# Kernel tuning notes

Measured on AMD Instinct MI355X. Metric: run time of the kernel, lower is better.

The kernel has to match this reference:

```python
import jax, jax.numpy as jnp
import numpy as np

# Model hyperparams (match init_kwargs)
B, T, CIN, COUT = 4, 12, 4, 4
P = 16; HIMG = WIMG = 256; HP = WP = 16
D = 384; L = 4; DFF = 4 * D; MAXG = 0.3
CPLX = jnp.complex64

# NOTE: RiemannianCliffordConv2d / TemporalPropagator / FluxTracker / basis /
# encoder / decoder sources were not provided; they are reconstructed here as
# faithful-structure surrogates: plain conv2d for the Clifford conv, complex
# linear eigen-basis encode/decode, exp-decay scan operators, complex FFN,
# patch-embed conv encoder and per-patch linear decoder. sde_mode='ode' so the
# stochastic branch is skipped, matching the explicit guard in the source.

def _ln(x, g, b):
    m = x.mean(-1, keepdims=True)
    v = jnp.var(x, axis=-1, keepdims=True)
    return (x - m) * jax.lax.rsqrt(v + 1e-5) * g + b

def _conv(x, w, b, stride, pad):
    y = jax.lax.conv_general_dilated(x, w, (stride, stride), pad,
                                     dimension_numbers=('NCHW', 'OIHW', 'NCHW'))
    return y + b[None, :, None, None]

def _pscan(A, X):
    # first-order linear recurrence h_t = A_t*h_{t-1} + X_t via associative scan over axis=1
    def comb(l, r):
        al, xl = l; ar, xr = r
        return al * ar, xl * ar + xr
    return jax.lax.associative_scan(comb, (A, X), axis=1)[1]

def _cgelu(z):
    return jax.nn.gelu(z.real) + 1j * jax.nn.gelu(z.imag)

def _model(x, dt, enc_w, enc_b, ns_g, ns_b, cw, cb, nt_g, nt_b,
           E_re, E_im, Ei_re, Ei_im, lam_flux, Ws_re, Ws_im, Wg, nu, omega,
           w1_re, w1_im, w2_re, w2_im, dec_w, dec_b):
    Bx, Tx = x.shape[0], x.shape[1]
    # ---- encoder: patch-embed conv -> complex latent (B,T,D,HP,WP)
    xf = x.reshape(Bx * Tx, CIN, HIMG, WIMG)
    e = _conv(xf, enc_w, enc_b, P, 'VALID')              # (BT, 2D, HP, WP)
    zr, zi = jnp.split(e, 2, axis=1)
    z = (zr + 1j * zi).astype(CPLX).reshape(Bx, Tx, D, HP, WP)
    for i in range(L):
        E = E_re[i] + 1j * E_im[i]
        Ei = Ei_re[i] + 1j * Ei_im[i]
        Ws = Ws_re[i] + 1j * Ws_im[i]
        W1 = w1_re[i] + 1j * w1_im[i]
        W2 = w2_re[i] + 1j * w2_im[i]
        # ---- _apply_spatial (residual Clifford conv on stacked re/im)
        xflat = z.reshape(Bx * Tx, D, HP, WP)
        xr2 = jnp.concatenate([xflat.real, xflat.imag], axis=1)   # (BT,2D,H,W)
        xn = jnp.transpose(xr2, (0, 2, 3, 1))
        xn = _ln(xn, ns_g[i], ns_b[i])
        xn = jnp.transpose(xn, (0, 3, 1, 2))
        xs = _conv(xn, cw[i], cb[i], 1, 'SAME')
        sre, sim = jnp.split(xs, 2, axis=1)
        xflat = xflat + (sre + 1j * sim)
        z = xflat.reshape(Bx, Tx, D, HP, WP)
        # ---- eigen-basis encode
        xp = jnp.transpose(z, (0, 1, 3, 4, 2))                    # (B,T,H,W,D)
        x_eig = jnp.einsum('bthwd,de->bthwe', xp, E)
        x_mean = x_eig.mean(axis=(2, 3))                          # (B,T,D)
        # ---- flux tracker scan (states start at zero => flux_prev term vanishes)
        a = jnp.exp(-jax.nn.softplus(lam_flux[i])[None, None] * dt[..., None])
        A_flux = a.astype(CPLX)
        X_flux = x_mean * dt[..., None]
        flux = _pscan(A_flux, X_flux)                             # (B,T,D) complex
        source = jnp.einsum('btd,de->bte', flux, Ws)
        gate = jax.nn.sigmoid(flux.real * Wg[i][None, None])      # (B,T,D) real
        g = gate[:, :, None, None, :]
        forcing = x_eig * g + source[:, :, None, None, :] * (1.0 - g)
        # ---- transition operators and temporal pscan
        lam = jnp.clip(-jax.nn.softplus(nu[i]), -5.0, MAXG) + 1j * omega[i]  # (D,)
        op_decay = jnp.exp(lam[None, None] * dt[..., None])       # (B,T,D) complex
        op_forcing = (op_decay - 1.0) / lam
        u_t = forcing * op_forcing[:, :, None, None, :]           # (B,T,H,W,D)
        # h_prev is zero-initialized per _init_states => its t0 contribution is zero
        A_full = jnp.broadcast_to(op_decay[:, :, None, None, :], u_t.shape)
        u_out = _pscan(A_full, u_t)                               # (B,T,H,W,D)
        # ---- decode + temporal FFN residual
        decoded = jnp.einsum('bthwd,de->bthwe', u_out, Ei)
        dec5 = jnp.transpose(decoded, (0, 1, 4, 2, 3))            # (B,T,D,H,W)
        df = dec5.reshape(Bx * Tx, D, HP, WP)
        dr = jnp.concatenate([df.real, df.imag], axis=1)
        dn = _ln(jnp.transpose(dr, (0, 2, 3, 1)), nt_g[i], nt_b[i])
        dn = jnp.transpose(dn, (0, 3, 1, 2))
        nre, nim = jnp.split(dn, 2, axis=1)
        xcl = jnp.transpose(nre + 1j * nim, (0, 2, 3, 1))          # (BT,H,W,D)
        delta = jnp.einsum('bhwf,fd->bhwd', _cgelu(jnp.einsum('bhwd,df->bhwf', xcl, W1)), W2)
        delta = jnp.transpose(delta, (0, 3, 1, 2))
        x_out = (df + delta).reshape(Bx, Tx, D, HP, WP)
        z = z + x_out
    # ---- ensemble decoder (mean member): per-patch linear head + depth-to-space
    feats = jnp.concatenate([z.real, z.imag], axis=2)             # (B,T,2D,H,W)
    fl = jnp.transpose(feats, (0, 1, 3, 4, 2))                    # (B,T,H,W,2D)
    y = jnp.einsum('bthwc,oc->bthwo', fl, dec_w) + dec_b
    y = y.reshape(Bx, Tx, HP, WP, COUT, P, P)
    y = jnp.transpose(y, (0, 1, 4, 2, 5, 3, 6)).reshape(Bx, Tx, COUT, HP * P, WP * P)
    return y


def setup_inputs() -> dict:
    key = jax.random.key(0)
    ks = jax.random.split(key, 32)
    s = 0.02
    d = {}
    d['x'] = jax.random.normal(ks[0], (B, T, CIN, HIMG, WIMG), dtype=jnp.float32)
    d['dt'] = jax.random.uniform(ks[1], (B, T), minval=0.5, maxval=1.5, dtype=jnp.float32)
    d['enc_w'] = jax.random.normal(ks[2], (2 * D, CIN, P, P), dtype=jnp.float32) * s
    d['enc_b'] = jnp.zeros((2 * D,), jnp.float32)
    d['ns_g'] = jnp.ones((L, 2 * D), jnp.float32)
    d['ns_b'] = jnp.zeros((L, 2 * D), jnp.float32)
    d['cw'] = jax.random.normal(ks[3], (L, 2 * D, 2 * D, 3, 3), dtype=jnp.float32) * s
    d['cb'] = jnp.zeros((L, 2 * D), jnp.float32)
    d['nt_g'] = jnp.ones((L, 2 * D), jnp.float32)
    d['nt_b'] = jnp.zeros((L, 2 * D), jnp.float32)
    d['E_re'] = jax.random.normal(ks[4], (L, D, D), dtype=jnp.float32) * s
    d['E_im'] = jax.random.normal(ks[5], (L, D, D), dtype=jnp.float32) * s
    d['Ei_re'] = jax.random.normal(ks[6], (L, D, D), dtype=jnp.float32) * s
    d['Ei_im'] = jax.random.normal(ks[7], (L, D, D), dtype=jnp.float32) * s
    d['lam_flux'] = jax.random.normal(ks[8], (L, D), dtype=jnp.float32)
    d['Ws_re'] = jax.random.normal(ks[9], (L, D, D), dtype=jnp.float32) * s
    d['Ws_im'] = jax.random.normal(ks[10], (L, D, D), dtype=jnp.float32) * s
    d['Wg'] = jax.random.normal(ks[11], (L, D), dtype=jnp.float32)
    d['nu'] = jax.random.normal(ks[12], (L, D), dtype=jnp.float32)
    d['omega'] = jax.random.normal(ks[13], (L, D), dtype=jnp.float32) * 0.5
    d['w1_re'] = jax.random.normal(ks[14], (L, D, DFF), dtype=jnp.float32) * s
    d['w1_im'] = jax.random.normal(ks[15], (L, D, DFF), dtype=jnp.float32) * s
    d['w2_re'] = jax.random.normal(ks[16], (L, DFF, D), dtype=jnp.float32) * s
    d['w2_im'] = jax.random.normal(ks[17], (L, DFF, D), dtype=jnp.float32) * s
    d['dec_w'] = jax.random.normal(ks[18], (COUT * P * P, 2 * D), dtype=jnp.float32) * s
    d['dec_b'] = jnp.zeros((COUT * P * P,), jnp.float32)
    return d


def reference(x, dt, enc_w, enc_b, ns_g, ns_b, cw, cb, nt_g, nt_b,
              E_re, E_im, Ei_re, Ei_im, lam_flux, Ws_re, Ws_im, Wg, nu, omega,
              w1_re, w1_im, w2_re, w2_im, dec_w, dec_b):
    return _model(x, dt, enc_w, enc_b, ns_g, ns_b, cw, cb, nt_g, nt_b,
                  E_re, E_im, Ei_re, Ei_im, lam_flux, Ws_re, Ws_im, Wg, nu, omega,
                  w1_re, w1_im, w2_re, w2_im, dec_w, dec_b)
```

## Files before the change

### kernel.cpp

```cpp
#include <hip/hip_runtime.h>
#include <cstddef>
#include <cstdint>

typedef unsigned short u16;
typedef short bf16x8 __attribute__((ext_vector_type(8)));
typedef float f32x4 __attribute__((ext_vector_type(4)));

__device__ __forceinline__ float gelu_tanh(float x) {
  float x3 = x * x * x;
  float t = tanhf(0.7978845608028654f * (x + 0.044715f * x3));
  return 0.5f * x * (1.0f + t);
}
__device__ __forceinline__ float softplus_f(float x) {
  return (x > 20.0f) ? x : log1pf(expf(x));
}
__device__ __forceinline__ u16 f2bf(float f) {
  uint32_t u = __float_as_uint(f);
  uint32_t r = (u + 0x7fffu + ((u >> 16) & 1u)) >> 16;
  return (u16)r;
}

__device__ __forceinline__ void gload16(const u16* g, u16* l) {
  __builtin_amdgcn_global_load_lds(
      (const __attribute__((address_space(1))) void*)g,
      (__attribute__((address_space(3))) void*)l, 16, 0, 0);
}

template <int MODE>
__global__ __launch_bounds__(256) void gemm128_kernel(
    const u16* __restrict__ A, const u16* __restrict__ Bt, int K, int ldc,
    float* __restrict__ Cf, u16* __restrict__ Cb, const float* __restrict__ bias) {
  __shared__ u16 As[128 * 32];
  __shared__ u16 Bs[128 * 32];
  const int m0 = blockIdx.x * 128, n0 = blockIdx.y * 128;
  const int tid = threadIdx.x;
  const int lane = tid & 63, w = tid >> 6;
  const int lane15 = lane & 15, quad = lane >> 4;
  const int r0 = lane >> 2, e0 = (lane & 3) * 8;

  const u16* ag0 = A + (size_t)(m0 + w * 32 + r0) * K + e0;
  const u16* ag1 = A + (size_t)(m0 + w * 32 + 16 + r0) * K + e0;
  const u16* bg0 = Bt + (size_t)(n0 + w * 32 + r0) * K + e0;
  const u16* bg1 = Bt + (size_t)(n0 + w * 32 + 16 + r0) * K + e0;
  u16* As0 = As + w * 1024; u16* As1 = As0 + 512;
  u16* Bs0 = Bs + w * 1024; u16* Bs1 = Bs0 + 512;

  f32x4 acc[4][4] = {};
  const int wy = w >> 1, wx = w & 1;
  const int ar_base = (wy * 64 + lane15) * 32 + quad * 8;
  const int br_base = (wx * 64 + lane15) * 32 + quad * 8;

  for (int k0 = 0; k0 < K; k0 += 32) {
    gload16(ag0 + k0, As0);
    gload16(ag1 + k0, As1);
    gload16(bg0 + k0, Bs0);
    gload16(bg1 + k0, Bs1);
    __syncthreads();
    bf16x8 af[4], bf[4];
#pragma unroll
    for (int i = 0; i < 4; ++i) af[i] = *(const bf16x8*)&As[ar_base + i * 16 * 32];
#pragma unroll
    for (int j = 0; j < 4; ++j) bf[j] = *(const bf16x8*)&Bs[br_base + j * 16 * 32];
#pragma unroll
    for (int i = 0; i < 4; ++i)
#pragma unroll
      for (int j = 0; j < 4; ++j)
        acc[i][j] = __builtin_amdgcn_mfma_f32_16x16x32_bf16(af[i], bf[j], acc[i][j], 0, 0, 0);
    __syncthreads();
  }

  const int mw = m0 + wy * 64, nw = n0 + wx * 64;
#pragma unroll
  for (int i = 0; i < 4; ++i) {
#pragma unroll
    for (int j = 0; j < 4; ++j) {
      const int col = nw + j * 16 + lane15;
#pragma unroll
      for (int r = 0; r < 4; ++r) {
        const int row = mw + i * 16 + quad * 4 + r;
        const float v = acc[i][j][r];
        if (MODE == 0) {
          Cf[(size_t)row * ldc + col] = v;
        } else if (MODE == 1) {
          Cb[(size_t)row * ldc + col] = f2bf(gelu_tanh(v));
        } else if (MODE == 2) {
          Cf[(size_t)row * ldc + col] += v;
        } else if (MODE == 3) {
          const int frame = row >> 8, pix = row & 255;
          const int hp = pix >> 4, wp = pix & 15;
          const int co = col >> 8, p1 = (col >> 4) & 15, p2 = col & 15;
          Cf[(((size_t)frame * 4 + co) * 256 + hp * 16 + p1) * 256 + wp * 16 + p2] = v + bias[col];
        }
      }
    }
  }
}

__global__ __launch_bounds__(256) void conv_mfma128_kernel(
    const u16* __restrict__ xnp, const u16* __restrict__ Btc,
    const float* __restrict__ cbias,
    float* __restrict__ z, u16* __restrict__ zb) {
  __shared__ u16 As[128 * 32];
  __shared__ u16 Bs[128 * 32];
  const int m0 = blockIdx.x * 128, n0 = blockIdx.y * 128;
  const int tid = threadIdx.x;
  const int lane = tid & 63, w = tid >> 6;
  const int lane15 = lane & 15, quad = lane >> 4;
  const int r0 = lane >> 2, e0 = (lane & 3) * 8;

  const int rowA0 = m0 + w * 32 + r0, rowA1 = rowA0 + 16;
  const long long cen0 = ((long long)(rowA0 >> 8) * 324 + ((((rowA0 & 255) >> 4) + 1) * 18) + (rowA0 & 15) + 1) * 768 + e0;
  const long long cen1 = ((long long)(rowA1 >> 8) * 324 + ((((rowA1 & 255) >> 4) + 1) * 18) + (rowA1 & 15) + 1) * 768 + e0;
  const u16* bg0 = Btc + (size_t)(n0 + w * 32 + r0) * 6912 + e0;
  const u16* bg1 = bg0 + (size_t)16 * 6912;
  u16* As0 = As + w * 1024; u16* As1 = As0 + 512;
  u16* Bs0 = Bs + w * 1024; u16* Bs1 = Bs0 + 512;

  f32x4 acc[4][4] = {};
  const int wy = w >> 1, wx = w & 1;
  const int ar_base = (wy * 64 + lane15) * 32 + quad * 8;
  const int br_base = (wx * 64 + lane15) * 32 + quad * 8;

  for (int tap = 0; tap < 9; ++tap) {
    const int doff = ((tap / 3 - 1) * 18 + (tap % 3 - 1)) * 768;
    const u16* a0 = xnp + cen0 + doff;
    const u16* a1 = xnp + cen1 + doff;
    const u16* b0 = bg0 + tap * 768;
    const u16* b1 = bg1 + tap * 768;
    for (int kc = 0; kc < 768; kc += 32) {
      gload16(a0 + kc, As0);
      gload16(a1 + kc, As1);
      gload16(b0 + kc, Bs0);
      gload16(b1 + kc, Bs1);
      __syncthreads();
      bf16x8 af[4], bf[4];
#pragma unroll
      for (int i = 0; i < 4; ++i) af[i] = *(const bf16x8*)&As[ar_base + i * 16 * 32];
#pragma unroll
      for (int j = 0; j < 4; ++j) bf[j] = *(const bf16x8*)&Bs[br_base + j * 16 * 32];
#pragma unroll
      for (int i = 0; i < 4; ++i)
#pragma unroll
        for (int j = 0; j < 4; ++j)
          acc[i][j] = __builtin_amdgcn_mfma_f32_16x16x32_bf16(af[i], bf[j], acc[i][j], 0, 0, 0);
      __syncthreads();
    }
  }

  const int mw = m0 + wy * 64, nw = n0 + wx * 64;
#pragma unroll
  for (int i = 0; i < 4; ++i) {
#pragma unroll
    for (int j = 0; j < 4; ++j) {
      const int col = nw + j * 16 + lane15;
      const float bv = cbias[col];
#pragma unroll
      for (int r = 0; r < 4; ++r) {
        const int row = mw + i * 16 + quad * 4 + r;
        const size_t idx = (size_t)row * 768 + col;
        const float nz = z[idx] + acc[i][j][r] + bv;
        z[idx] = nz;
        zb[idx] = f2bf(nz);
      }
    }
  }
}

__global__ __launch_bounds__(256) void encoder_mfma_kernel(
    const float* __restrict__ x, const float* __restrict__ ew,
    const float* __restrict__ eb, float* __restrict__ z) {
  __shared__ u16 As[128 * 32];
  __shared__ u16 Bs[128 * 32];
  const int m0 = blockIdx.x * 128, n0 = blockIdx.y * 128;
  const int tid = threadIdx.x;
  const int lane = tid & 63, w = tid >> 6;
  const int lane15 = lane & 15, quad = lane >> 4;
  const int srow = tid >> 1, half = tid & 1;
  const int arow = m0 + srow;
  const int frame = arow >> 8, pix = arow & 255, hh = pix >> 4, ww = pix & 15;

  f32x4 acc[4][4] = {};
  const int wy = w >> 1, wx = w & 1;
  const int ar_base = (wy * 64 + lane15) * 32 + quad * 8;
  const int br_base = (wx * 64 + lane15) * 32 + quad * 8;

  for (int k0 = 0; k0 < 1024; k0 += 32) {
    const int gk = k0 + half * 16;
    const int c = gk >> 8, ph = (gk >> 4) & 15;
    const float* ax = x + (((size_t)(frame * 4 + c) * 256 + hh * 16 + ph) * 256 + ww * 16);
    const float* bx = ew + (size_t)(n0 + srow) * 1024 + gk;
    u16 ta[16], tb[16];
#pragma unroll
    for (int j = 0; j < 4; ++j) {
      const float4 va = *(const float4*)(ax + j * 4);
      const float4 vb = *(const float4*)(bx + j * 4);
      ta[j * 4 + 0] = f2bf(va.x); ta[j * 4 + 1] = f2bf(va.y);
      ta[j * 4 + 2] = f2bf(va.z); ta[j * 4 + 3] = f2bf(va.w);
      tb[j * 4 + 0] = f2bf(vb.x); tb[j * 4 + 1] = f2bf(vb.y);
      tb[j * 4 + 2] = f2bf(vb.z); tb[j * 4 + 3] = f2bf(vb.w);
    }
    __syncthreads();
    *(uint4*)&As[srow * 32 + half * 16] = *(uint4*)ta;
    *(uint4*)&As[srow * 32 + half * 16 + 8] = *(uint4*)(ta + 8);
    *(uint4*)&Bs[srow * 32 + half * 16] = *(uint4*)tb;
    *(uint4*)&Bs[srow * 32 + half * 16 + 8] = *(uint4*)(tb + 8);
    __syncthreads();
    bf16x8 af[4], bfv[4];
#pragma unroll
    for (int i = 0; i < 4; ++i) af[i] = *(const bf16x8*)&As[ar_base + i * 16 * 32];
#pragma unroll
    for (int j = 0; j < 4; ++j) bfv[j] = *(const bf16x8*)&Bs[br_base + j * 16 * 32];
#pragma unroll
    for (int i = 0; i < 4; ++i)
#pragma unroll
      for (int j = 0; j < 4; ++j)
        acc[i][j] = __builtin_amdgcn_mfma_f32_16x16x32_bf16(af[i], bfv[j], acc[i][j], 0, 0, 0);
  }

  const int mw = m0 + wy * 64, nw = n0 + wx * 64;
#pragma unroll
  for (int i = 0; i < 4; ++i)
#pragma unroll
    for (int j = 0; j < 4; ++j) {
      const int col = nw + j * 16 + lane15;
      const float bv = eb[col];
#pragma unroll
      for (int r = 0; r < 4; ++r) {
        const int row = mw + i * 16 + quad * 4 + r;
        z[(size_t)row * 768 + col] = acc[i][j][r] + bv;
      }
    }
}

__global__ __launch_bounds__(256) void expand_kernel(
    const float* __restrict__ Wre, const float* __restrict__ Wim,
    int ldw, int Kc, int Nc, u16* __restrict__ Wt) {
  __shared__ float tile[32][33];
  const int k0 = blockIdx.x * 32, n0 = blockIdx.y * 32;
  const bool khi = k0 >= Kc, nhi = n0 >= Nc;
  const float* src = (khi != nhi) ? Wim : Wre;
  const float sgn = (!nhi && khi) ? -1.0f : 1.0f;
  const int sk = k0 - (khi ? Kc : 0), sn = n0 - (nhi ? Nc : 0);
  const int c = threadIdx.x & 31, r8 = threadIdx.x >> 5;
  for (int r = r8; r < 32; r += 8)
    tile[r][c] = src[(size_t)(sk + r) * ldw + sn + c];
  __syncthreads();
  const int twoK = 2 * Kc;
  for (int r = r8; r < 32; r += 8)
    Wt[(size_t)(n0 + r) * twoK + k0 + c] = f2bf(sgn * tile[c][r]);
}

__global__ __launch_bounds__(256) void reorder_cw_kernel(
    const float* __restrict__ cwl, u16* __restrict__ Btc) {
  __shared__ float buf[6912];
  const int o = blockIdx.x;
  const float* src = cwl + (size_t)o * 6912;
  for (int i = threadIdx.x; i < 6912; i += 256) buf[i] = src[i];
  __syncthreads();
  u16* dst = Btc + (size_t)o * 6912;
  for (int i = threadIdx.x; i < 6912; i += 256) {
    const int tap = i / 768, cc = i - tap * 768;
    dst[i] = f2bf(buf[cc * 9 + tap]);
  }
}

__global__ __launch_bounds__(256) void cast_bf16_kernel(
    const float* __restrict__ in, u16* __restrict__ out, int n) {
  const int g = blockIdx.x * 256 + threadIdx.x;
  if (g < n) out[g] = f2bf(in[g]);
}

template <bool HALO>
__global__ __launch_bounds__(192) void ln_kernel(
    const float* __restrict__ in, const float* __restrict__ g,
    const float* __restrict__ b, u16* __restrict__ out) {
  const int row = blockIdx.x, tid = threadIdx.x;
  const float4 v = *(const float4*)(in + (size_t)row * 768 + tid * 4);
  float s = v.x + v.y + v.z + v.w;
  float q = v.x * v.x + v.y * v.y + v.z * v.z + v.w * v.w;
#pragma unroll
  for (int off = 32; off > 0; off >>= 1) {
    s += __shfl_down(s, off);
    q += __shfl_down(q, off);
  }
  __shared__ float rs[3], rq[3];
  if ((tid & 63) == 0) { rs[tid >> 6] = s; rq[tid >> 6] = q; }
  __syncthreads();
  const float S = rs[0] + rs[1] + rs[2], Q = rq[0] + rq[1] + rq[2];
  const float mean = S * (1.0f / 768.0f);
  const float inv = rsqrtf(Q * (1.0f / 768.0f) - mean * mean + 1e-5f);
  const float4 gv = *(const float4*)(g + tid * 4);
  const float4 bv = *(const float4*)(b + tid * 4);
  u16 p[4];
  p[0] = f2bf((v.x - mean) * inv * gv.x + bv.x);
  p[1] = f2bf((v.y - mean) * inv * gv.y + bv.y);
  p[2] = f2bf((v.z - mean) * inv * gv.z + bv.z);
  p[3] = f2bf((v.w - mean) * inv * gv.w + bv.w);
  size_t base;
  if (HALO) {
    const int f = row >> 8, pp = row & 255, h = pp >> 4, ww = pp & 15;
    base = ((size_t)f * 324 + (h + 1) * 18 + ww + 1) * 768;
  } else {
    base = (size_t)row * 768;
  }
  *(uint2*)(out + base + tid * 4) = *(uint2*)p;
}

__global__ __launch_bounds__(768) void mean_kernel(
    const float* __restrict__ eig, float* __restrict__ mr, float* __restrict__ mi) {
  const int f = blockIdx.x, c = threadIdx.x;
  const float* p = eig + (size_t)f * 256 * 768 + c;
  float s0 = 0.f, s1 = 0.f, s2 = 0.f, s3 = 0.f;
  for (int px = 0; px < 256; px += 4) {
    s0 += p[(size_t)px * 768];
    s1 += p[(size_t)(px + 1) * 768];
    s2 += p[(size_t)(px + 2) * 768];
    s3 += p[(size_t)(px + 3) * 768];
  }
  const float tot = (s0 + s1 + s2 + s3) * (1.0f / 256.0f);
  if (c < 384) mr[f * 384 + c] = tot;
  else         mi[f * 384 + c - 384] = tot;
}

__global__ __launch_bounds__(384) void flux_kernel(
    const float* __restrict__ dt, const float* __restrict__ lamf,
    const float* __restrict__ nu, const float* __restrict__ omega,
    const float* __restrict__ mr, const float* __restrict__ mi,
    float* __restrict__ fluxr, float* __restrict__ fluxi,
    float* __restrict__ opdr, float* __restrict__ opdi,
    float* __restrict__ opfr, float* __restrict__ opfi) {
  const int b = blockIdx.x;
  const int d = threadIdx.x;
  const float sp = softplus_f(lamf[d]);
  float lre = -softplus_f(nu[d]);
  lre = fmaxf(lre, -5.0f);
  const float lim = omega[d];
  const float den = lre * lre + lim * lim;
  float fr = 0.f, fi = 0.f;
  for (int t = 0; t < 12; ++t) {
    const float dtv = dt[b * 12 + t];
    const int idx = (b * 12 + t) * 384 + d;
    const float A = expf(-sp * dtv);
    fr = A * fr + mr[idx] * dtv;
    fi = A * fi + mi[idx] * dtv;
    fluxr[idx] = fr; fluxi[idx] = fi;
    const float ed = expf(lre * dtv);
    const float odr = ed * cosf(lim * dtv);
    const float odi = ed * sinf(lim * dtv);
    opdr[idx] = odr; opdi[idx] = odi;
    const float nr_ = odr - 1.0f, ni_ = odi;
    opfr[idx] = (nr_ * lre + ni_ * lim) / den;
    opfi[idx] = (ni_ * lre - nr_ * lim) / den;
  }
}

#define SBM 64
#define SBN 64
#define SBK 32
__global__ __launch_bounds__(256) void cgemm_small_kernel(
    const float* __restrict__ Ar, const float* __restrict__ Ai, int lda,
    const float* __restrict__ Wr, const float* __restrict__ Wi, int ldw,
    float* __restrict__ Cr, float* __restrict__ Ci, int ldc, int M, int K) {
  __shared__ float Asr[SBK][SBM], Asi[SBK][SBM];
  __shared__ float Wsr[SBK][SBN], Wsi[SBK][SBN];
  const int m0 = blockIdx.x * SBM;
  const int n0 = blockIdx.y * SBN;
  const int tid = threadIdx.x;
  const int tn = tid & 15, tm = tid >> 4;
  float accr[4][4] = {}, acci[4][4] = {};
  for (int k0 = 0; k0 < K; k0 += SBK) {
    for (int s = tid; s < 512; s += 256) {
      {
        int r = s >> 3, kk = (s & 7) << 2;
        int row = m0 + r;
        float4 vr = {0.f, 0.f, 0.f, 0.f}, vi = {0.f, 0.f, 0.f, 0.f};
        if (row < M) {
          vr = *(const float4*)(Ar + (size_t)row * lda + k0 + kk);
          vi = *(const float4*)(Ai + (size_t)row * lda + k0 + kk);
        }
        Asr[kk + 0][r] = vr.x; Asr[kk + 1][r] = vr.y; Asr[kk + 2][r] = vr.z; Asr[kk + 3][r] = vr.w;
        Asi[kk + 0][r] = vi.x; Asi[kk + 1][r] = vi.y; Asi[kk + 2][r] = vi.z; Asi[kk + 3][r] = vi.w;
      }
      {
        int wr_ = s >> 4, wc = (s & 15) << 2;
        *(float4*)&Wsr[wr_][wc] = *(const float4*)(Wr + (size_t)(k0 + wr_) * ldw + n0 + wc);
        *(float4*)&Wsi[wr_][wc] = *(const float4*)(Wi + (size_t)(k0 + wr_) * ldw + n0 + wc);
      }
    }
    __syncthreads();
#pragma unroll
    for (int kk = 0; kk < SBK; ++kk) {
      float4 ar4 = *(const float4*)&Asr[kk][tm << 2];
      float4 ai4 = *(const float4*)&Asi[kk][tm << 2];
      float4 wr4 = *(const float4*)&Wsr[kk][tn << 2];
      float4 wi4 = *(const float4*)&Wsi[kk][tn << 2];
      float ar[4] = {ar4.x, ar4.y, ar4.z, ar4.w};
      float ai[4] = {ai4.x, ai4.y, ai4.z, ai4.w};
      float wr[4] = {wr4.x, wr4.y, wr4.z, wr4.w};
      float wi[4] = {wi4.x, wi4.y, wi4.z, wi4.w};
#pragma unroll
      for (int i = 0; i < 4; ++i)
#pragma unroll
        for (int j = 0; j < 4; ++j) {
          accr[i][j] = fmaf(ar[i], wr[j], accr[i][j]);
          accr[i][j] = fmaf(-ai[i], wi[j], accr[i][j]);
          acci[i][j] = fmaf(ar[i], wi[j], acci[i][j]);
          acci[i][j] = fmaf(ai[i], wr[j], acci[i][j]);
        }
    }
    __syncthreads();
  }
#pragma unroll
  for (int i = 0; i < 4; ++i) {
    int row = m0 + (tm << 2) + i;
    if (row >= M) continue;
#pragma unroll
    for (int j = 0; j < 4; ++j) {
      int col = n0 + (tn << 2) + j;
      size_t idx = (size_t)row * ldc + col;
      Cr[idx] = accr[i][j]; Ci[idx] = acci[i][j];
    }
  }
}

__global__ __launch_bounds__(256) void forcing_kernel(
    float* __restrict__ eig, const float* __restrict__ fluxr,
    const float* __restrict__ srcr, const float* __restrict__ srci,
    const float* __restrict__ Wg,
    const float* __restrict__ opfr, const float* __restrict__ opfi) {
  const int g = blockIdx.x * 256 + threadIdx.x;
  if (g >= 12288 * 384) return;
  const int d = g % 384;
  const int row = g / 384;
  const int fidx = (row >> 8) * 384 + d;
  const float gate = 1.0f / (1.0f + expf(-fluxr[fidx] * Wg[d]));
  const size_t ir = (size_t)row * 768 + d;
  const float er = eig[ir], ei = eig[ir + 384];
  const float fr = er * gate + srcr[fidx] * (1.0f - gate);
  const float fi = ei * gate + srci[fidx] * (1.0f - gate);
  const float pr = opfr[fidx], pi = opfi[fidx];
  eig[ir] = fr * pr - fi * pi;
  eig[ir + 384] = fr * pi + fi * pr;
}

__global__ __launch_bounds__(256) void pscan_u_kernel(
    const float* __restrict__ eig,
    const float* __restrict__ opdr, const float* __restrict__ opdi,
    u16* __restrict__ ub) {
  const int g = blockIdx.x * 256 + threadIdx.x;
  if (g >= 4 * 256 * 384) return;
  const int d = g % 384;
  const int pix = (g / 384) & 255;
  const int b = g / (384 * 256);
  float ur = 0.f, ui = 0.f;
  for (int t = 0; t < 12; ++t) {
    const int frame = b * 12 + t;
    const size_t idx = ((size_t)frame * 256 + pix) * 768 + d;
    const int fidx = frame * 384 + d;
    const float ar = opdr[fidx], ai = opdi[fidx];
    const float nr = ar * ur - ai * ui + eig[idx];
    const float ni = ar * ui + ai * ur + eig[idx + 384];
    ub[idx] = f2bf(nr); ub[idx + 384] = f2bf(ni);
    ur = nr; ui = ni;
  }
}

__global__ __launch_bounds__(256) void add_df_kernel(
    float* __restrict__ z, const float* __restrict__ df, int n4) {
  const int g = blockIdx.x * 256 + threadIdx.x;
  if (g < n4) {
    float4 a = *(const float4*)(z + (size_t)g * 4);
    const float4 b = *(const float4*)(df + (size_t)g * 4);
    a.x += b.x; a.y += b.y; a.z += b.z; a.w += b.w;
    *(float4*)(z + (size_t)g * 4) = a;
  }
}

extern "C" void kernel_launch(void* const* d_in, const int* in_sizes, int n_in,
                              void* d_out, int out_size, void* d_ws, size_t ws_size,
                              hipStream_t stream) {
  const float* x        = (const float*)d_in[0];
  const float* dt       = (const float*)d_in[1];
  const float* enc_w    = (const float*)d_in[2];
  const float* enc_b    = (const float*)d_in[3];
  const float* ns_g     = (const float*)d_in[4];
  const float* ns_b     = (const float*)d_in[5];
  const float* cw       = (const float*)d_in[6];
  const float* cb       = (const float*)d_in[7];
  const float* nt_g     = (const float*)d_in[8];
  const float* nt_b     = (const float*)d_in[9];
  const float* E_re     = (const float*)d_in[10];
  const float* E_im     = (const float*)d_in[11];
  const float* Ei_re    = (const float*)d_in[12];
  const float* Ei_im    = (const float*)d_in[13];
  const float* lam_flux = (const float*)d_in[14];
  const float* Ws_re    = (const float*)d_in[15];
  const float* Ws_im    = (const float*)d_in[16];
  const float* Wg       = (const float*)d_in[17];
  const float* nu       = (const float*)d_in[18];
  const float* omega    = (const float*)d_in[19];
  const float* w1_re    = (const float*)d_in[20];
  const float* w1_im    = (const float*)d_in[21];
  const float* w2_re    = (const float*)d_in[22];
  const float* w2_im    = (const float*)d_in[23];
  const float* dec_w    = (const float*)d_in[24];
  const float* dec_b    = (const float*)d_in[25];
  float* out = (float*)d_out;

  const size_t NPF = 12288ull * 768;
  const size_t XNP = 48ull * 324 * 768;
  const size_t SM = 48ull * 384;

  float* z   = (float*)d_ws;
  float* eig = z + NPF;
  float* df  = eig + NPF;
  u16* xnp   = (u16*)(df + NPF);
  u16* Btc   = xnp + XNP;
  u16* Et    = Btc + 5308416;
  u16* Eit   = Et + 589824;
  u16* W1t   = Eit + 589824;
  u16* W2t   = W1t + 2359296;
  u16* dwt   = W2t + 2359296;
  float* sm  = (float*)(dwt + 786432);
  float* mr    = sm;            float* mi    = mr + SM;
  float* fluxr = mi + SM;       float* fluxi = fluxr + SM;
  float* opdr  = fluxi + SM;    float* opdi  = opdr + SM;
  float* opfr  = opdi + SM;     float* opfi  = opfr + SM;
  float* srcr  = opfi + SM;     float* srci  = srcr + SM;

  const size_t need = ((char*)(srci + SM)) - ((char*)d_ws);
  if (ws_size < need) return;

  u16* zb  = (u16*)df;
  u16* h1b = (u16*)eig;

  cast_bf16_kernel<<<(786432 + 255) / 256, 256, 0, stream>>>(dec_w, dwt, 786432);

  encoder_mfma_kernel<<<dim3(96, 6), 256, 0, stream>>>(x, enc_w, enc_b, z);

  for (int l = 0; l < 4; ++l) {
    const size_t DD = 384ull * 384, DF = 384ull * 1536;
    hipMemsetAsync(xnp, 0, XNP * sizeof(u16), stream);
    reorder_cw_kernel<<<768, 256, 0, stream>>>(cw + (size_t)l * 768 * 768 * 9, Btc);
    expand_kernel<<<dim3(24, 24), 256, 0, stream>>>(E_re + l * DD, E_im + l * DD, 384, 384, 384, Et);
    expand_kernel<<<dim3(24, 24), 256, 0, stream>>>(Ei_re + l * DD, Ei_im + l * DD, 384, 384, 384, Eit);
    for (int ch = 0; ch < 2; ++ch) {
      expand_kernel<<<dim3(24, 48), 256, 0, stream>>>(
          w1_re + l * DF + ch * 768, w1_im + l * DF + ch * 768, 1536, 384, 768, W1t + (size_t)ch * 1179648);
      expand_kernel<<<dim3(48, 24), 256, 0, stream>>>(
          w2_re + l * DF + (size_t)ch * 768 * 384, w2_im + l * DF + (size_t)ch * 768 * 384, 384, 768, 384,
          W2t + (size_t)ch * 1179648);
    }

    ln_kernel<true><<<12288, 192, 0, stream>>>(z, ns_g + l * 768, ns_b + l * 768, xnp);
    conv_mfma128_kernel<<<dim3(96, 6), 256, 0, stream>>>(xnp, Btc, cb + l * 768, z, zb);
    gemm128_kernel<0><<<dim3(96, 6), 256, 0, stream>>>(zb, Et, 768, 768, eig, nullptr, nullptr);
    mean_kernel<<<48, 768, 0, stream>>>(eig, mr, mi);
    flux_kernel<<<4, 384, 0, stream>>>(dt, lam_flux + l * 384, nu + l * 384, omega + l * 384,
                                       mr, mi, fluxr, fluxi, opdr, opdi, opfr, opfi);
    cgemm_small_kernel<<<dim3(1, 6), 256, 0, stream>>>(
        fluxr, fluxi, 384, Ws_re + l * DD, Ws_im + l * DD, 384, srcr, srci, 384, 48, 384);
    forcing_kernel<<<(12288 * 384 + 255) / 256, 256, 0, stream>>>(
        eig, fluxr, srcr, srci, Wg + l * 384, opfr, opfi);
    pscan_u_kernel<<<1536, 256, 0, stream>>>(eig, opdr, opdi, xnp);
    gemm128_kernel<0><<<dim3(96, 6), 256, 0, stream>>>(xnp, Eit, 768, 768, df, nullptr, nullptr);
    ln_kernel<false><<<12288, 192, 0, stream>>>(df, nt_g + l * 768, nt_b + l * 768, xnp);
    add_df_kernel<<<(int)((NPF / 4 + 255) / 256), 256, 0, stream>>>(z, df, (int)(NPF / 4));
    for (int ch = 0; ch < 2; ++ch) {
      gemm128_kernel<1><<<dim3(96, 12), 256, 0, stream>>>(
          xnp, W1t + (size_t)ch * 1179648, 768, 1536, nullptr, h1b, nullptr);
      gemm128_kernel<2><<<dim3(96, 6), 256, 0, stream>>>(
          h1b, W2t + (size_t)ch * 1179648, 1536, 768, z, nullptr, nullptr);
    }
  }

  cast_bf16_kernel<<<(int)((NPF + 255) / 256), 256, 0, stream>>>(z, zb, (int)NPF);
  gemm128_kernel<3><<<dim3(96, 8), 256, 0, stream>>>(zb, dwt, 768, 0, out, nullptr, dec_b);
}
```

Baseline: 2.954 ms.

## Retile GEMMs to 128x64 with 64-wide K steps and fuse elementwise kernels

The GEMM and conv kernels get a template N-tile of 64 for most N=768 GEMMs, which doubles the block count to 1152. Each barrier now loads two 32-wide K slices, halving the syncs per K. The forcing step is split: the gate and source terms are computed in the small complex GEMM epilogue, and the per-pixel part is folded into the scan kernel. The df residual add is folded into the first W2 GEMM epilogue, and the final bf16 cast into the last W2 GEMM. This removes several full-tensor elementwise passes and launches, at the cost of more LDS per block and smaller per-wave tiles with less register reuse.

```diff
diff --git a/kernel.cpp b/kernel.cpp
--- a/kernel.cpp
+++ b/kernel.cpp
@@ -26,52 +26,65 @@
       (__attribute__((address_space(3))) void*)l, 16, 0, 0);
 }
 
-template <int MODE>
-__global__ __launch_bounds__(256) void gemm128_kernel(
+template <int TN, int MODE>
+__global__ __launch_bounds__(256) void gemm_kernel(
     const u16* __restrict__ A, const u16* __restrict__ Bt, int K, int ldc,
-    float* __restrict__ Cf, u16* __restrict__ Cb, const float* __restrict__ bias) {
-  __shared__ u16 As[128 * 32];
-  __shared__ u16 Bs[128 * 32];
-  const int m0 = blockIdx.x * 128, n0 = blockIdx.y * 128;
+    float* __restrict__ Cf, u16* __restrict__ Cb,
+    const float* __restrict__ bias, const float* __restrict__ Df) {
+  __shared__ u16 As[2][128 * 32];
+  __shared__ u16 Bs[2][TN * 32];
+  constexpr int NI = (TN == 64) ? 2 : 4;
+  const int m0 = blockIdx.x * 128, n0 = blockIdx.y * TN;
   const int tid = threadIdx.x;
   const int lane = tid & 63, w = tid >> 6;
   const int lane15 = lane & 15, quad = lane >> 4;
   const int r0 = lane >> 2, e0 = (lane & 3) * 8;
+  const int wy = (TN == 64) ? w : (w >> 1);
+  const int wx = (TN == 64) ? 0 : (w & 1);
 
   const u16* ag0 = A + (size_t)(m0 + w * 32 + r0) * K + e0;
-  const u16* ag1 = A + (size_t)(m0 + w * 32 + 16 + r0) * K + e0;
-  const u16* bg0 = Bt + (size_t)(n0 + w * 32 + r0) * K + e0;
-  const u16* bg1 = Bt + (size_t)(n0 + w * 32 + 16 + r0) * K + e0;
-  u16* As0 = As + w * 1024; u16* As1 = As0 + 512;
-  u16* Bs0 = Bs + w * 1024; u16* Bs1 = Bs0 + 512;
-
-  f32x4 acc[4][4] = {};
-  const int wy = w >> 1, wx = w & 1;
-  const int ar_base = (wy * 64 + lane15) * 32 + quad * 8;
-  const int br_base = (wx * 64 + lane15) * 32 + quad * 8;
-
-  for (int k0 = 0; k0 < K; k0 += 32) {
-    gload16(ag0 + k0, As0);
-    gload16(ag1 + k0, As1);
-    gload16(bg0 + k0, Bs0);
-    gload16(bg1 + k0, Bs1);
+  const u16* ag1 = ag0 + (size_t)16 * K;
+  const u16* bg0 = (TN == 64) ? Bt + (size_t)(n0 + w * 16 + r0) * K + e0
+                              : Bt + (size_t)(n0 + w * 32 + r0) * K + e0;
+  const u16* bg1 = bg0 + (size_t)16 * K;
+
+  f32x4 acc[NI][4] = {};
+  const int abase = (wy * (16 * NI) + lane15) * 32 + quad * 8;
+  const int bbase = (wx * 64 + lane15) * 32 + quad * 8;
+
+  for (int k0 = 0; k0 < K; k0 += 64) {
+#pragma unroll
+    for (int p = 0; p < 2; ++p) {
+      const int kk = k0 + 32 * p;
+      gload16(ag0 + kk, &As[p][w * 1024]);
+      gload16(ag1 + kk, &As[p][w * 1024 + 512]);
+      if (TN == 64) {
+        gload16(bg0 + kk, &Bs[p][w * 512]);
+      } else {
+        gload16(bg0 + kk, &Bs[p][w * 1024]);
+        gload16(bg1 + kk, &Bs[p][w * 1024 + 512]);
+      }
+    }
     __syncthreads();
-    bf16x8 af[4], bf[4];
-#pragma unroll
-    for (int i = 0; i < 4; ++i) af[i] = *(const bf16x8*)&As[ar_base + i * 16 * 32];
-#pragma unroll
-    for (int j = 0; j < 4; ++j) bf[j] = *(const bf16x8*)&Bs[br_base + j * 16 * 32];
-#pragma unroll
-    for (int i = 0; i < 4; ++i)
-#pragma unroll
-      for (int j = 0; j < 4; ++j)
-        acc[i][j] = __builtin_amdgcn_mfma_f32_16x16x32_bf16(af[i], bf[j], acc[i][j], 0, 0, 0);
+#pragma unroll
+    for (int p = 0; p < 2; ++p) {
+      bf16x8 af[NI], bf[4];
+#pragma unroll
+      for (int i = 0; i < NI; ++i) af[i] = *(const bf16x8*)&As[p][abase + i * 16 * 32];
+#pragma unroll
+      for (int j = 0; j < 4; ++j) bf[j] = *(const bf16x8*)&Bs[p][bbase + j * 16 * 32];
+#pragma unroll
+      for (int i = 0; i < NI; ++i)
+#pragma unroll
+        for (int j = 0; j < 4; ++j)
+          acc[i][j] = __builtin_amdgcn_mfma_f32_16x16x32_bf16(af[i], bf[j], acc[i][j], 0, 0, 0);
+    }
     __syncthreads();
   }
 
-  const int mw = m0 + wy * 64, nw = n0 + wx * 64;
-#pragma unroll
-  for (int i = 0; i < 4; ++i) {
+  const int mw = m0 + wy * (16 * NI), nw = n0 + wx * 64;
+#pragma unroll
+  for (int i = 0; i < NI; ++i) {
 #pragma unroll
     for (int j = 0; j < 4; ++j) {
       const int col = nw + j * 16 + lane15;
@@ -79,30 +92,37 @@
       for (int r = 0; r < 4; ++r) {
         const int row = mw + i * 16 + quad * 4 + r;
         const float v = acc[i][j][r];
+        const size_t idx = (size_t)row * ldc + col;
         if (MODE == 0) {
-          Cf[(size_t)row * ldc + col] = v;
+          Cf[idx] = v;
         } else if (MODE == 1) {
-          Cb[(size_t)row * ldc + col] = f2bf(gelu_tanh(v));
+          Cb[idx] = f2bf(gelu_tanh(v));
         } else if (MODE == 2) {
-          Cf[(size_t)row * ldc + col] += v;
+          Cf[idx] += v;
         } else if (MODE == 3) {
           const int frame = row >> 8, pix = row & 255;
           const int hp = pix >> 4, wp = pix & 15;
           const int co = col >> 8, p1 = (col >> 4) & 15, p2 = col & 15;
           Cf[(((size_t)frame * 4 + co) * 256 + hp * 16 + p1) * 256 + wp * 16 + p2] = v + bias[col];
+        } else if (MODE == 4) {
+          Cf[idx] += v + Df[idx];
+        } else if (MODE == 5) {
+          const float nz = Cf[idx] + v;
+          Cf[idx] = nz;
+          Cb[idx] = f2bf(nz);
         }
       }
     }
   }
 }
 
-__global__ __launch_bounds__(256) void conv_mfma128_kernel(
+__global__ __launch_bounds__(256) void conv_mfma_kernel(
     const u16* __restrict__ xnp, const u16* __restrict__ Btc,
     const float* __restrict__ cbias,
     float* __restrict__ z, u16* __restrict__ zb) {
-  __shared__ u16 As[128 * 32];
-  __shared__ u16 Bs[128 * 32];
-  const int m0 = blockIdx.x * 128, n0 = blockIdx.y * 128;
+  __shared__ u16 As[2][128 * 32];
+  __shared__ u16 Bs[2][64 * 32];
+  const int m0 = blockIdx.x * 128, n0 = blockIdx.y * 64;
   const int tid = threadIdx.x;
   const int lane = tid & 63, w = tid >> 6;
   const int lane15 = lane & 15, quad = lane >> 4;
@@ -111,48 +131,49 @@
   const int rowA0 = m0 + w * 32 + r0, rowA1 = rowA0 + 16;
   const long long cen0 = ((long long)(rowA0 >> 8) * 324 + ((((rowA0 & 255) >> 4) + 1) * 18) + (rowA0 & 15) + 1) * 768 + e0;
   const long long cen1 = ((long long)(rowA1 >> 8) * 324 + ((((rowA1 & 255) >> 4) + 1) * 18) + (rowA1 & 15) + 1) * 768 + e0;
-  const u16* bg0 = Btc + (size_t)(n0 + w * 32 + r0) * 6912 + e0;
-  const u16* bg1 = bg0 + (size_t)16 * 6912;
-  u16* As0 = As + w * 1024; u16* As1 = As0 + 512;
-  u16* Bs0 = Bs + w * 1024; u16* Bs1 = Bs0 + 512;
-
-  f32x4 acc[4][4] = {};
-  const int wy = w >> 1, wx = w & 1;
-  const int ar_base = (wy * 64 + lane15) * 32 + quad * 8;
-  const int br_base = (wx * 64 + lane15) * 32 + quad * 8;
+  const u16* bg = Btc + (size_t)(n0 + w * 16 + r0) * 6912 + e0;
+
+  f32x4 acc[2][4] = {};
+  const int abase = (w * 32 + lane15) * 32 + quad * 8;
+  const int bbase = (lane15) * 32 + quad * 8;
 
   for (int tap = 0; tap < 9; ++tap) {
     const int doff = ((tap / 3 - 1) * 18 + (tap % 3 - 1)) * 768;
     const u16* a0 = xnp + cen0 + doff;
     const u16* a1 = xnp + cen1 + doff;
-    const u16* b0 = bg0 + tap * 768;
-    const u16* b1 = bg1 + tap * 768;
-    for (int kc = 0; kc < 768; kc += 32) {
-      gload16(a0 + kc, As0);
-      gload16(a1 + kc, As1);
-      gload16(b0 + kc, Bs0);
-      gload16(b1 + kc, Bs1);
+    const u16* b0 = bg + tap * 768;
+    for (int kc = 0; kc < 768; kc += 64) {
+#pragma unroll
+      for (int p = 0; p < 2; ++p) {
+        const int kk = kc + 32 * p;
+        gload16(a0 + kk, &As[p][w * 1024]);
+        gload16(a1 + kk, &As[p][w * 1024 + 512]);
+        gload16(b0 + kk, &Bs[p][w * 512]);
+      }
       __syncthreads();
-      bf16x8 af[4], bf[4];
-#pragma unroll
-      for (int i = 0; i < 4; ++i) af[i] = *(const bf16x8*)&As[ar_base + i * 16 * 32];
-#pragma unroll
-      for (int j = 0; j < 4; ++j) bf[j] = *(const bf16x8*)&Bs[br_base + j * 16 * 32];
-#pragma unroll
-      for (int i = 0; i < 4; ++i)
-#pragma unroll
-        for (int j = 0; j < 4; ++j)
-          acc[i][j] = __builtin_amdgcn_mfma_f32_16x16x32_bf16(af[i], bf[j], acc[i][j], 0, 0, 0);
+#pragma unroll
+      for (int p = 0; p < 2; ++p) {
+        bf16x8 af[2], bf[4];
+#pragma unroll
+        for (int i = 0; i < 2; ++i) af[i] = *(const bf16x8*)&As[p][abase + i * 16 * 32];
+#pragma unroll
+        for (int j = 0; j < 4; ++j) bf[j] = *(const bf16x8*)&Bs[p][bbase + j * 16 * 32];
+#pragma unroll
+        for (int i = 0; i < 2; ++i)
+#pragma unroll
+          for (int j = 0; j < 4; ++j)
+            acc[i][j] = __builtin_amdgcn_mfma_f32_16x16x32_bf16(af[i], bf[j], acc[i][j], 0, 0, 0);
+      }
       __syncthreads();
     }
   }
 
-  const int mw = m0 + wy * 64, nw = n0 + wx * 64;
-#pragma unroll
-  for (int i = 0; i < 4; ++i) {
+  const int mw = m0 + w * 32;
+#pragma unroll
+  for (int i = 0; i < 2; ++i) {
 #pragma unroll
     for (int j = 0; j < 4; ++j) {
-      const int col = nw + j * 16 + lane15;
+      const int col = n0 + j * 16 + lane15;
       const float bv = cbias[col];
 #pragma unroll
       for (int r = 0; r < 4; ++r) {
@@ -357,10 +378,12 @@
 #define SBM 64
 #define SBN 64
 #define SBK 32
-__global__ __launch_bounds__(256) void cgemm_small_kernel(
+__global__ __launch_bounds__(256) void cgemm_src_kernel(
     const float* __restrict__ Ar, const float* __restrict__ Ai, int lda,
     const float* __restrict__ Wr, const float* __restrict__ Wi, int ldw,
-    float* __restrict__ Cr, float* __restrict__ Ci, int ldc, int M, int K) {
+    const float* __restrict__ Wg,
+    float* __restrict__ G, float* __restrict__ SGr, float* __restrict__ SGi,
+    int ldc, int M, int K) {
   __shared__ float Asr[SBK][SBM], Asi[SBK][SBM];
   __shared__ float Wsr[SBK][SBN], Wsi[SBK][SBN];
   const int m0 = blockIdx.x * SBM;
@@ -418,33 +441,19 @@
     for (int j = 0; j < 4; ++j) {
       int col = n0 + (tn << 2) + j;
       size_t idx = (size_t)row * ldc + col;
-      Cr[idx] = accr[i][j]; Ci[idx] = acci[i][j];
-    }
-  }
-}
-
-__global__ __launch_bounds__(256) void forcing_kernel(
-    float* __restrict__ eig, const float* __restrict__ fluxr,
-    const float* __restrict__ srcr, const float* __restrict__ srci,
-    const float* __restrict__ Wg,
-    const float* __restrict__ opfr, const float* __restrict__ opfi) {
-  const int g = blockIdx.x * 256 + threadIdx.x;
-  if (g >= 12288 * 384) return;
-  const int d = g % 384;
-  const int row = g / 384;
-  const int fidx = (row >> 8) * 384 + d;
-  const float gate = 1.0f / (1.0f + expf(-fluxr[fidx] * Wg[d]));
-  const size_t ir = (size_t)row * 768 + d;
-  const float er = eig[ir], ei = eig[ir + 384];
-  const float fr = er * gate + srcr[fidx] * (1.0f - gate);
-  const float fi = ei * gate + srci[fidx] * (1.0f - gate);
-  const float pr = opfr[fidx], pi = opfi[fidx];
-  eig[ir] = fr * pr - fi * pi;
-  eig[ir + 384] = fr * pi + fi * pr;
-}
-
-__global__ __launch_bounds__(256) void pscan_u_kernel(
+      const float gate = 1.0f / (1.0f + expf(- Ar[idx] * Wg[col]));
+      G[idx] = gate;
+      SGr[idx] = accr[i][j] * (1.0f - gate);
+      SGi[idx] = acci[i][j] * (1.0f - gate);
+    }
+  }
+}
+
+__global__ __launch_bounds__(256) void pscan_fused_kernel(
     const float* __restrict__ eig,
+    const float* __restrict__ Gv,
+    const float* __restrict__ SGr, const float* __restrict__ SGi,
+    const float* __restrict__ opfr, const float* __restrict__ opfi,
     const float* __restrict__ opdr, const float* __restrict__ opdi,
     u16* __restrict__ ub) {
   const int g = blockIdx.x * 256 + threadIdx.x;
@@ -457,22 +466,17 @@
     const int frame = b * 12 + t;
     const size_t idx = ((size_t)frame * 256 + pix) * 768 + d;
     const int fidx = frame * 384 + d;
+    const float G = Gv[fidx];
+    const float fr = eig[idx] * G + SGr[fidx];
+    const float fi = eig[idx + 384] * G + SGi[fidx];
+    const float pr = opfr[fidx], pi = opfi[fidx];
+    const float utr = fr * pr - fi * pi;
+    const float uti = fr * pi + fi * pr;
     const float ar = opdr[fidx], ai = opdi[fidx];
-    const float nr = ar * ur - ai * ui + eig[idx];
-    const float ni = ar * ui + ai * ur + eig[idx + 384];
+    const float nr = ar * ur - ai * ui + utr;
+    const float ni = ar * ui + ai * ur + uti;
     ub[idx] = f2bf(nr); ub[idx + 384] = f2bf(ni);
     ur = nr; ui = ni;
-  }
-}
-
-__global__ __launch_bounds__(256) void add_df_kernel(
-    float* __restrict__ z, const float* __restrict__ df, int n4) {
-  const int g = blockIdx.x * 256 + threadIdx.x;
-  if (g < n4) {
-    float4 a = *(const float4*)(z + (size_t)g * 4);
-    const float4 b = *(const float4*)(df + (size_t)g * 4);
-    a.x += b.x; a.y += b.y; a.z += b.z; a.w += b.w;
-    *(float4*)(z + (size_t)g * 4) = a;
   }
 }
 
@@ -526,16 +530,16 @@
   float* fluxr = mi + SM;       float* fluxi = fluxr + SM;
   float* opdr  = fluxi + SM;    float* opdi  = opdr + SM;
   float* opfr  = opdi + SM;     float* opfi  = opfr + SM;
-  float* srcr  = opfi + SM;     float* srci  = srcr + SM;
-
-  const size_t need = ((char*)(srci + SM)) - ((char*)d_ws);
+  float* Gv    = opfi + SM;     float* SGr   = Gv + SM;
+  float* SGi   = SGr + SM;
+
+  const size_t need = ((char*)(SGi + SM)) - ((char*)d_ws);
   if (ws_size < need) return;
 
   u16* zb  = (u16*)df;
   u16* h1b = (u16*)eig;
 
   cast_bf16_kernel<<<(786432 + 255) / 256, 256, 0, stream>>>(dec_w, dwt, 786432);
-
   encoder_mfma_kernel<<<dim3(96, 6), 256, 0, stream>>>(x, enc_w, enc_b, z);
 
   for (int l = 0; l < 4; ++l) {
@@ -553,27 +557,32 @@
     }
 
     ln_kernel<true><<<12288, 192, 0, stream>>>(z, ns_g + l * 768, ns_b + l * 768, xnp);
-    conv_mfma128_kernel<<<dim3(96, 6), 256, 0, stream>>>(xnp, Btc, cb + l * 768, z, zb);
-    gemm128_kernel<0><<<dim3(96, 6), 256, 0, stream>>>(zb, Et, 768, 768, eig, nullptr, nullptr);
+    conv_mfma_kernel<<<dim3(96, 12), 256, 0, stream>>>(xnp, Btc, cb + l * 768, z, zb);
+    gemm_kernel<64, 0><<<dim3(96, 12), 256, 0, stream>>>(zb, Et, 768, 768, eig, nullptr, nullptr, nullptr);
     mean_kernel<<<48, 768, 0, stream>>>(eig, mr, mi);
     flux_kernel<<<4, 384, 0, stream>>>(dt, lam_flux + l * 384, nu + l * 384, omega + l * 384,
                                        mr, mi, fluxr, fluxi, opdr, opdi, opfr, opfi);
-    cgemm_small_kernel<<<dim3(1, 6), 256, 0, stream>>>(
-        fluxr, fluxi, 384, Ws_re + l * DD, Ws_im + l * DD, 384, srcr, srci, 384, 48, 384);
-    forcing_kernel<<<(12288 * 384 + 255) / 256, 256, 0, stream>>>(
-        eig, fluxr, srcr, srci, Wg + l * 384, opfr, opfi);
-    pscan_u_kernel<<<1536, 256, 0, stream>>>(eig, opdr, opdi, xnp);
-    gemm128_kernel<0><<<dim3(96, 6), 256, 0, stream>>>(xnp, Eit, 768, 768, df, nullptr, nullptr);
+    cgemm_src_kernel<<<dim3(1, 6), 256, 0, stream>>>(
+        fluxr, fluxi, 384, Ws_re + l * DD, Ws_im + l * DD, 384,
+        Wg + l * 384, Gv, SGr, SGi, 384, 48, 384);
+    pscan_fused_kernel<<<1536, 256, 0, stream>>>(eig, Gv, SGr, SGi, opfr, opfi, opdr, opdi, xnp);
+    gemm_kernel<64, 0><<<dim3(96, 12), 256, 0, stream>>>(xnp, Eit, 768, 768, df, nullptr, nullptr, nullptr);
     ln_kernel<false><<<12288, 192, 0, stream>>>(df, nt_g + l * 768, nt_b + l * 768, xnp);
-    add_df_kernel<<<(int)((NPF / 4 + 255) / 256), 256, 0, stream>>>(z, df, (int)(NPF / 4));
     for (int ch = 0; ch < 2; ++ch) {
-      gemm128_kernel<1><<<dim3(96, 12), 256, 0, stream>>>(
-          xnp, W1t + (size_t)ch * 1179648, 768, 1536, nullptr, h1b, nullptr);
-      gemm128_kernel<2><<<dim3(96, 6), 256, 0, stream>>>(
-          h1b, W2t + (size_t)ch * 1179648, 1536, 768, z, nullptr, nullptr);
-    }
-  }
-
-  cast_bf16_kernel<<<(int)((NPF + 255) / 256), 256, 0, stream>>>(z, zb, (int)NPF);
-  gemm128_kernel<3><<<dim3(96, 8), 256, 0, stream>>>(zb, dwt, 768, 0, out, nullptr, dec_b);
-}
+      gemm_kernel<128, 1><<<dim3(96, 12), 256, 0, stream>>>(
+          xnp, W1t + (size_t)ch * 1179648, 768, 1536, nullptr, h1b, nullptr, nullptr);
+      if (ch == 0) {
+        gemm_kernel<64, 4><<<dim3(96, 12), 256, 0, stream>>>(
+            h1b, W2t, 1536, 768, z, nullptr, nullptr, df);
+      } else if (l < 3) {
+        gemm_kernel<64, 2><<<dim3(96, 12), 256, 0, stream>>>(
+            h1b, W2t + 1179648, 1536, 768, z, nullptr, nullptr, nullptr);
+      } else {
+        gemm_kernel<64, 5><<<dim3(96, 12), 256, 0, stream>>>(
+            h1b, W2t + 1179648, 1536, 768, z, zb, nullptr, nullptr);
+      }
+    }
+  }
+
+  gemm_kernel<64, 3><<<dim3(96, 16), 256, 0, stream>>>(zb, dwt, 768, 0, out, nullptr, dec_b, nullptr);
+}
```

Result: no change. 2.926 ms (-1.0%).
